# Kernel optimization log

Measured on AMD Instinct MI355X. Metric: run time of the kernel, lower is better.

## Reference

```python
import jax, jax.numpy as jnp
import numpy as np
import math

B, T, D, H, V = 32, 512, 256, 4, 5000
NL = 6          # transformer layers
DUR_CAP = 8     # cap per-token duration so output length is static under jit
T_OUT = 2048    # fixed regulated length (avg duration ~1-2 with small init)


def _layernorm(x, g, b, eps=1e-5):
    m = jnp.mean(x, axis=-1, keepdims=True)
    v = jnp.var(x, axis=-1, keepdims=True)
    return (x - m) * jax.lax.rsqrt(v + eps) * g + b


def _conv1d(x, w, b):
    # x [B,C,T], w [O,I,K] -> [B,O,T], 'same' padding as in torch
    pad = (w.shape[-1] - 1) // 2
    y = jax.lax.conv_general_dilated(x, w, (1,), [(pad, pad)],
                                     dimension_numbers=('NCH', 'OIH', 'NCH'))
    return y + b[None, :, None]


def _pos_encoding(t, d):
    pos = jnp.arange(t, dtype=jnp.float32)[:, None]
    div = jnp.exp(jnp.arange(0, d, 2, dtype=jnp.float32) * (-math.log(10000.0) / d))
    ang = pos * div  # [t, d/2]
    return jnp.stack([jnp.sin(ang), jnp.cos(ang)], axis=-1).reshape(t, d)


def setup_inputs():
    key = jax.random.key(0)
    ks = iter(jax.random.split(key, 64))
    def nrm(shape, s=0.02):
        return jax.random.normal(next(ks), shape, dtype=jnp.float32) * s
    return {
        'text': jax.random.randint(next(ks), (B, T), 0, V, dtype=jnp.int32),
        'emotion': jax.random.normal(next(ks), (B, 1), dtype=jnp.float32),
        'emb': nrm((V, D), 1.0),
        'Wqkv': nrm((NL, D, 3 * D)), 'bqkv': jnp.zeros((NL, 3 * D)),
        'Wo': nrm((NL, D, D)), 'bo': jnp.zeros((NL, D)),
        'W1': nrm((NL, D, 4 * D)), 'b1': jnp.zeros((NL, 4 * D)),
        'W2': nrm((NL, 4 * D, D)), 'b2': jnp.zeros((NL, D)),
        'ln1g': jnp.ones((NL, D)), 'ln1b': jnp.zeros((NL, D)),
        'ln2g': jnp.ones((NL, D)), 'ln2b': jnp.zeros((NL, D)),
        'We1': nrm((1, 64), 0.1), 'be1': jnp.zeros((64,)),
        'We2': nrm((64, D), 0.1), 'be2': jnp.zeros((D,)),
        'dp_w1': nrm((D, D, 3)), 'dp_b1': jnp.zeros((D,)),
        'dp_g1': jnp.ones((D,)), 'dp_bt1': jnp.zeros((D,)),
        'dp_m1': jnp.zeros((D,)), 'dp_v1': jnp.ones((D,)),
        'dp_w2': nrm((D, D, 3)), 'dp_b2': jnp.zeros((D,)),
        'dp_g2': jnp.ones((D,)), 'dp_bt2': jnp.zeros((D,)),
        'dp_m2': jnp.zeros((D,)), 'dp_v2': jnp.ones((D,)),
        'dp_wo': nrm((1, D, 1)), 'dp_bo': jnp.zeros((1,)),
        'dec_w1': nrm((256, D, 5)), 'dec_b1': jnp.zeros((256,)),
        'dec_w2': nrm((128, 256, 5)), 'dec_b2': jnp.zeros((128,)),
        'dec_w3': nrm((1, 128, 5)), 'dec_b3': jnp.zeros((1,)),
    }


def reference(text, emotion, emb, Wqkv, bqkv, Wo, bo, W1, b1, W2, b2,
              ln1g, ln1b, ln2g, ln2b, We1, be1, We2, be2,
              dp_w1, dp_b1, dp_g1, dp_bt1, dp_m1, dp_v1,
              dp_w2, dp_b2, dp_g2, dp_bt2, dp_m2, dp_v2, dp_wo, dp_bo,
              dec_w1, dec_b1, dec_w2, dec_b2, dec_w3, dec_b3):
    dh = D // H
    scale = 1.0 / math.sqrt(dh)
    x = emb[text] + _pos_encoding(T, D)[None]  # [B,T,D]
    # post-norm TransformerEncoder (torch default), relu FFN, eval mode
    for i in range(NL):
        qkv = x @ Wqkv[i] + bqkv[i]
        q, k, v = jnp.split(qkv, 3, axis=-1)
        q = q.reshape(B, T, H, dh); k = k.reshape(B, T, H, dh); v = v.reshape(B, T, H, dh)
        att = jax.nn.softmax(jnp.einsum('bthd,bshd->bhts', q, k) * scale, axis=-1)
        o = jnp.einsum('bhts,bshd->bthd', att, v).reshape(B, T, D) @ Wo[i] + bo[i]
        x = _layernorm(x + o, ln1g[i], ln1b[i])
        ff = jax.nn.relu(x @ W1[i] + b1[i]) @ W2[i] + b2[i]
        x = _layernorm(x + ff, ln2g[i], ln2b[i])
    # EmotionFusion (assumed additive MLP projection, output_dim = 256)
    e = jax.nn.relu(emotion @ We1 + be1) @ We2 + be2  # [B,256]
    fused = x + e[:, None, :]                          # [B,T,D]
    # DurationPredictor (eval: BN with running stats, dropout off)
    def bn(y, g, bt, m, vv):
        return g[None, :, None] * (y - m[None, :, None]) * jax.lax.rsqrt(vv + 1e-5)[None, :, None] + bt[None, :, None]
    h = fused.transpose(0, 2, 1)  # [B,D,T]
    h = bn(jax.nn.relu(_conv1d(h, dp_w1, dp_b1)), dp_g1, dp_bt1, dp_m1, dp_v1)
    h = bn(jax.nn.relu(_conv1d(h, dp_w2, dp_b2)), dp_g2, dp_bt2, dp_m2, dp_v2)
    log_dur = _conv1d(h, dp_wo, dp_bo)[:, 0, :]  # [B,T]
    dur = jnp.clip(jnp.round(jnp.exp(log_dur)), 1, DUR_CAP).astype(jnp.int32)
    dur = jax.lax.stop_gradient(dur)
    # LengthRegulator: repeat token i dur[i] times, zero-pad to T_OUT
    def regulate(xb, db):
        total = jnp.sum(db)
        pad = jnp.maximum(T_OUT - total, 0)
        xe = jnp.concatenate([xb, jnp.zeros((1, D), xb.dtype)], axis=0)
        de = jnp.concatenate([db, pad[None]], axis=0)
        return jnp.repeat(xe, de, axis=0, total_repeat_length=T_OUT)
    reg = jax.vmap(regulate)(fused, dur)  # [B,T_OUT,D]
    # decoder conv stack
    y = reg.transpose(0, 2, 1)
    y = jax.nn.relu(_conv1d(y, dec_w1, dec_b1))
    y = jax.nn.relu(_conv1d(y, dec_w2, dec_b2))
    wav = _conv1d(y, dec_w3, dec_b3)[:, 0, :]  # [B,T_OUT]
    return wav
```

## Files before the change

kernel.cpp:

```cpp
#include <hip/hip_runtime.h>
#include <math.h>

#define NB 32
#define NT 512
#define ND 256
#define NH 4
#define NLAYER 6
#define TOUT 2048

typedef __attribute__((ext_vector_type(8))) short bf16x8;
typedef __attribute__((ext_vector_type(4))) float f32x4;
typedef __attribute__((ext_vector_type(16))) float f32x16;

static __device__ __forceinline__ unsigned short f2b(float f) {
    union { float f; unsigned int u; } x; x.f = f;
    unsigned int u = x.u;
    return (unsigned short)((u + 0x7FFFu + ((u >> 16) & 1u)) >> 16);
}
static __device__ __forceinline__ float b2f(unsigned short s) {
    union { unsigned int u; float f; } x; x.u = ((unsigned int)s) << 16;
    return x.f;
}

#define OFF_X    0ull
#define OFF_FFH  4194304ull
#define OFF_WBT  12582912ull
#define OFF_CWT  14942208ull
#define OFF_QKV  20971520ull
#define OFF_ATTN 33554432ull
#define OFF_PROJ 37748736ull
#define OFF_E    41943040ull
#define OFF_INT  41951232ull

__global__ __launch_bounds__(256) void embed_kernel(const int* __restrict__ text,
                                                    const float* __restrict__ emb,
                                                    float* __restrict__ x)
{
    const int row = blockIdx.x;
    const int d = threadIdx.x;
    const int t = row & (NT - 1);
    const int id = text[row];
    const int j2 = (d >> 1) * 2;
    const float c = -9.210340371976184f / 256.0f;
    float freq = expf((float)j2 * c);
    float ang = (float)t * freq;
    float pe = (d & 1) ? cosf(ang) : sinf(ang);
    x[(size_t)row * ND + d] = emb[(size_t)id * ND + d] + pe;
}

__global__ __launch_bounds__(256) void wq_kernel(const float* __restrict__ W,
                                                 unsigned short* __restrict__ out,
                                                 int K, int N, int inLS, int outLS)
{
    __shared__ float tile[32][33];
    const float* Wl = W + (size_t)blockIdx.z * inLS;
    unsigned short* ol = out + (size_t)blockIdx.z * outLS;
    const int n0 = blockIdx.x * 32, k0 = blockIdx.y * 32;
    const int tx = threadIdx.x & 31, ty = threadIdx.x >> 5;
#pragma unroll
    for (int j = 0; j < 4; ++j)
        tile[ty + j * 8][tx] = Wl[(size_t)(k0 + ty + j * 8) * N + n0 + tx];
    __syncthreads();
#pragma unroll
    for (int j = 0; j < 4; ++j)
        ol[(size_t)(n0 + ty + j * 8) * K + k0 + tx] = f2b(tile[tx][ty + j * 8]);
}

template<int NTILE, bool RELU, bool ABF16, bool CBF16>
__global__ __launch_bounds__(256) void gemmbf_kernel(const void* __restrict__ A_,
                                                     const unsigned short* __restrict__ Bt,
                                                     const float* __restrict__ bias,
                                                     void* __restrict__ C_,
                                                     int M, int N, int K)
{
    constexpr int MT = (NTILE == 128) ? 2 : 1;
    __shared__ __align__(16) unsigned short Asb[128 * 32];
    __shared__ __align__(16) unsigned short Bsb[NTILE * 32];
    const int tid = threadIdx.x;
    const int lane = tid & 63, wave = tid >> 6;
    const int ln = lane & 31, hi = lane >> 5;
    const int row0 = blockIdx.y * 128, col0 = blockIdx.x * NTILE;
    const int mOff = (NTILE == 128) ? (wave >> 1) * 64 : wave * 32;
    const int nOff = (NTILE == 128) ? (wave & 1) * 64 : 0;
    const float* Af = (const float*)A_;
    const unsigned short* Ab = (const unsigned short*)A_;
    float* Cf = (float*)C_;
    unsigned short* Cb = (unsigned short*)C_;
    f32x16 acc[MT][2] = {};

    for (int k0 = 0; k0 < K; k0 += 32) {
#pragma unroll
        for (int it = 0; it < 2; ++it) {
            int u = it * 256 + tid;
            int m = u >> 2, blk = u & 3;
            unsigned short s8[8];
            if (ABF16) {
                *(uint4*)s8 = *(const uint4*)&Ab[(size_t)(row0 + m) * K + k0 + blk * 8];
            } else {
                float4 v0 = *(const float4*)&Af[(size_t)(row0 + m) * K + k0 + blk * 8];
                float4 v1 = *(const float4*)&Af[(size_t)(row0 + m) * K + k0 + blk * 8 + 4];
                s8[0] = f2b(v0.x); s8[1] = f2b(v0.y); s8[2] = f2b(v0.z); s8[3] = f2b(v0.w);
                s8[4] = f2b(v1.x); s8[5] = f2b(v1.y); s8[6] = f2b(v1.z); s8[7] = f2b(v1.w);
            }
            *(uint4*)&Asb[m * 32 + ((blk ^ (m & 3)) << 3)] = *(uint4*)s8;
        }
#pragma unroll
        for (int it = 0; it < NTILE / 64; ++it) {
            int u = it * 256 + tid;
            int n = u >> 2, blk = u & 3;
            *(uint4*)&Bsb[n * 32 + ((blk ^ (n & 3)) << 3)] =
                *(const uint4*)&Bt[(size_t)(col0 + n) * K + k0 + blk * 8];
        }
        __syncthreads();
#pragma unroll
        for (int kh = 0; kh < 2; ++kh) {
            const int kb = kh * 2 + hi;
            bf16x8 af[MT], bfr[2];
#pragma unroll
            for (int mt = 0; mt < MT; ++mt) {
                int r = mOff + mt * 32 + ln;
                af[mt] = *(const bf16x8*)&Asb[r * 32 + ((kb ^ (r & 3)) << 3)];
            }
#pragma unroll
            for (int nt = 0; nt < 2; ++nt) {
                int r = nOff + nt * 32 + ln;
                bfr[nt] = *(const bf16x8*)&Bsb[r * 32 + ((kb ^ (r & 3)) << 3)];
            }
#pragma unroll
            for (int mt = 0; mt < MT; ++mt)
#pragma unroll
                for (int nt = 0; nt < 2; ++nt)
                    acc[mt][nt] = __builtin_amdgcn_mfma_f32_32x32x16_bf16(
                        af[mt], bfr[nt], acc[mt][nt], 0, 0, 0);
        }
        __syncthreads();
    }
#pragma unroll
    for (int mt = 0; mt < MT; ++mt)
#pragma unroll
        for (int nt = 0; nt < 2; ++nt) {
            int col = col0 + nOff + nt * 32 + ln;
            float bi = bias[col];
#pragma unroll
            for (int g = 0; g < 4; ++g)
#pragma unroll
                for (int r4 = 0; r4 < 4; ++r4) {
                    int row = row0 + mOff + mt * 32 + hi * 4 + g * 8 + r4;
                    float v = acc[mt][nt][g * 4 + r4] + bi;
                    if (RELU) v = fmaxf(v, 0.f);
                    if (CBF16) Cb[(size_t)row * N + col] = f2b(v);
                    else       Cf[(size_t)row * N + col] = v;
                }
        }
}

__global__ __launch_bounds__(256) void vtrans_kernel(const unsigned short* __restrict__ qkv,
                                                     unsigned short* __restrict__ vt)
{
    __shared__ unsigned short tile[64][65];
    const int t0 = blockIdx.x * 64, h = blockIdx.y, b = blockIdx.z;
    const int tid = threadIdx.x;
#pragma unroll
    for (int it = 0; it < 2; ++it) {
        int u = it * 256 + tid;
        int t = u >> 3, d8 = (u & 7) * 8;
        bf16x8 v = *(const bf16x8*)&qkv[((size_t)(b * NT) + t0 + t) * 768 + 512 + h * 64 + d8];
#pragma unroll
        for (int j = 0; j < 8; ++j) tile[t][d8 + j] = (unsigned short)v[j];
    }
    __syncthreads();
#pragma unroll
    for (int it = 0; it < 2; ++it) {
        int u = it * 256 + tid;
        int d = u >> 3, t8 = (u & 7) * 8;
        unsigned short s8[8];
#pragma unroll
        for (int j = 0; j < 8; ++j) s8[j] = tile[t8 + j][d];
        *(uint4*)&vt[((size_t)(b * NH + h) * 64 + d) * NT + t0 + t8] = *(uint4*)s8;
    }
}

__global__ __launch_bounds__(256, 2) void attn3_kernel(const unsigned short* __restrict__ qkv,
                                                       const unsigned short* __restrict__ vt,
                                                       unsigned short* __restrict__ out)
{
    __shared__ __align__(16) unsigned short sP[4][32 * 64];
    const int tid = threadIdx.x;
    const int lane = tid & 63, wave = tid >> 6;
    const int ln = lane & 31, hi = lane >> 5;
    const int h = blockIdx.y, b = blockIdx.z;
    const int q0 = blockIdx.x * 128 + wave * 32;
    const size_t base = (size_t)b * NT * 768;
    const int qoff = h * 64;
    const unsigned short* vbh = vt + (size_t)(b * NH + h) * 64 * NT;

    bf16x8 qf[4];
#pragma unroll
    for (int s = 0; s < 4; ++s)
        qf[s] = *(const bf16x8*)&qkv[base + (size_t)(q0 + ln) * 768 + qoff + s * 16 + hi * 8];

    float mrow[16], lrow[16];
#pragma unroll
    for (int i = 0; i < 16; ++i) { mrow[i] = -1e30f; lrow[i] = 0.f; }
    f32x16 oacc[2] = {};
    const float sc = 0.18033688011112042f;
    const int i0 = (ln & 3) | (((ln >> 3) & 3) << 2);
    const bool own = (((ln >> 2) & 1) == hi);
    unsigned short* Pw = &sP[wave][0];

    for (int ch = 0; ch < 8; ++ch) {
        const int s0 = ch * 64;
        f32x16 sacc[2] = {};
#pragma unroll
        for (int ct = 0; ct < 2; ++ct)
#pragma unroll
            for (int s = 0; s < 4; ++s) {
                bf16x8 kf = *(const bf16x8*)&qkv[base + (size_t)(s0 + ct * 32 + ln) * 768
                                                 + 256 + qoff + s * 16 + hi * 8];
                sacc[ct] = __builtin_amdgcn_mfma_f32_32x32x16_bf16(qf[s], kf, sacc[ct], 0, 0, 0);
            }
        float alpha[16];
#pragma unroll
        for (int i = 0; i < 16; ++i) {
            float s20 = sacc[0][i] * sc, s21 = sacc[1][i] * sc;
            float mx = fmaxf(s20, s21);
#pragma unroll
            for (int o = 1; o < 32; o <<= 1) mx = fmaxf(mx, __shfl_xor(mx, o));
            float mn = fmaxf(mrow[i], mx);
            alpha[i] = exp2f(mrow[i] - mn);
            mrow[i] = mn;
            float p0 = exp2f(s20 - mn);
            float p1 = exp2f(s21 - mn);
            sacc[0][i] = p0; sacc[1][i] = p1;
            float rs = p0 + p1;
#pragma unroll
            for (int o = 1; o < 32; o <<= 1) rs += __shfl_xor(rs, o);
            lrow[i] = lrow[i] * alpha[i] + rs;
        }
#pragma unroll
        for (int ct = 0; ct < 2; ++ct) {
            int kb = ct * 4 + (ln >> 3), k7 = ln & 7;
#pragma unroll
            for (int i = 0; i < 16; ++i) {
                int q = (i & 3) + 8 * (i >> 2) + 4 * hi;
                Pw[q * 64 + (((kb ^ (q & 7)) << 3) | k7)] = f2b(sacc[ct][i]);
            }
        }
        __syncthreads();
        {
            float av = alpha[i0];
            float ao = __shfl_xor(av, 32);
            float aq = own ? av : ao;
#pragma unroll
            for (int ct = 0; ct < 2; ++ct)
#pragma unroll
                for (int i = 0; i < 16; ++i)
                    oacc[ct][i] *= aq;
        }
#pragma unroll
        for (int s = 0; s < 4; ++s) {
            bf16x8 pf = *(const bf16x8*)&Pw[ln * 64 + (((s * 2 + hi) ^ (ln & 7)) << 3)];
#pragma unroll
            for (int ct = 0; ct < 2; ++ct) {
                bf16x8 vf = *(const bf16x8*)&vbh[(size_t)(ct * 32 + ln) * NT + s0 + s * 16 + hi * 8];
                oacc[ct] = __builtin_amdgcn_mfma_f32_32x32x16_bf16(vf, pf, oacc[ct], 0, 0, 0);
            }
        }
        __syncthreads();
    }
    float lv = lrow[i0];
    float lo = __shfl_xor(lv, 32);
    float linv = 1.0f / (own ? lv : lo);
    const int q = q0 + ln;
#pragma unroll
    for (int ct = 0; ct < 2; ++ct)
#pragma unroll
        for (int i = 0; i < 16; ++i) {
            int d = ct * 32 + (i & 3) + 8 * (i >> 2) + 4 * hi;
            out[(size_t)(b * NT + q) * ND + qoff + d] = f2b(oacc[ct][i] * linv);
        }
}

__global__ __launch_bounds__(256) void add_ln_kernel(float* __restrict__ x,
                                                     const float* __restrict__ y,
                                                     const float* __restrict__ g,
                                                     const float* __restrict__ bta)
{
    const int w = threadIdx.x >> 6, lane = threadIdx.x & 63;
    const size_t row = (size_t)blockIdx.x * 4 + w;
    const int c4 = lane * 4;
    float4 xv = *(const float4*)&x[row * ND + c4];
    float4 yv = *(const float4*)&y[row * ND + c4];
    float4 v = make_float4(xv.x + yv.x, xv.y + yv.y, xv.z + yv.z, xv.w + yv.w);
    float s = v.x + v.y + v.z + v.w;
#pragma unroll
    for (int o = 1; o < 64; o <<= 1) s += __shfl_xor(s, o);
    float m = s * (1.0f / 256.0f);
    float4 dv = make_float4(v.x - m, v.y - m, v.z - m, v.w - m);
    float s2 = dv.x * dv.x + dv.y * dv.y + dv.z * dv.z + dv.w * dv.w;
#pragma unroll
    for (int o = 1; o < 64; o <<= 1) s2 += __shfl_xor(s2, o);
    float r = 1.0f / sqrtf(s2 * (1.0f / 256.0f) + 1e-5f);
    float4 gv = *(const float4*)&g[c4];
    float4 bv = *(const float4*)&bta[c4];
    float4 o4 = make_float4(dv.x * r * gv.x + bv.x, dv.y * r * gv.y + bv.y,
                            dv.z * r * gv.z + bv.z, dv.w * r * gv.w + bv.w);
    *(float4*)&x[row * ND + c4] = o4;
}

__global__ __launch_bounds__(256) void emotion_kernel(const float* __restrict__ emo,
                                                      const float* __restrict__ We1,
                                                      const float* __restrict__ be1,
                                                      const float* __restrict__ We2,
                                                      const float* __restrict__ be2,
                                                      float* __restrict__ e)
{
    const int b = blockIdx.x, d = threadIdx.x;
    const float em = emo[b];
    float acc = be2[d];
    for (int j = 0; j < 64; ++j) {
        float h = fmaxf(em * We1[j] + be1[j], 0.0f);
        acc = fmaf(h, We2[j * ND + d], acc);
    }
    e[b * ND + d] = acc;
}

__global__ __launch_bounds__(256) void addfuse_kernel(float* __restrict__ x,
                                                      const float* __restrict__ e)
{
    const int row = blockIdx.x;
    const int d = threadIdx.x;
    x[(size_t)row * ND + d] += e[(row >> 9) * ND + d];
}

__global__ __launch_bounds__(256) void wtrans_kernel(const float* __restrict__ w,
                                                     float* __restrict__ wt,
                                                     int CIN, int COUT, int KS)
{
    int gid = blockIdx.x * 256 + threadIdx.x;
    int total = CIN * COUT * KS;
    if (gid >= total) return;
    int o = gid % COUT;
    int r = gid / COUT;
    int c = r % CIN;
    int k = r / CIN;
    wt[gid] = w[(o * CIN + c) * KS + k];
}

__global__ __launch_bounds__(256) void wtransb_kernel(const float* __restrict__ w,
                                                      unsigned short* __restrict__ wtb,
                                                      int CIN, int COUT, int KS)
{
    int gid = blockIdx.x * 256 + threadIdx.x;
    int total = CIN * COUT * KS;
    if (gid >= total) return;
    int c = gid % CIN;
    int r = gid / CIN;
    int o = r % COUT;
    int k = r / COUT;
    wtb[gid] = f2b(w[(o * CIN + c) * KS + k]);
}

template<int CIN, int KS, bool RELU, bool BN, bool GATHER>
__global__ __launch_bounds__(256, 4) void convg_kernel(const float* __restrict__ in,
                                                       const float* __restrict__ wt,
                                                       const float* __restrict__ bias,
                                                       const float* __restrict__ bng,
                                                       const float* __restrict__ bnb,
                                                       const float* __restrict__ bnm,
                                                       const float* __restrict__ bnv,
                                                       const int* __restrict__ tok,
                                                       float* __restrict__ out,
                                                       int T, int in_T, int COUT)
{
    constexpr int TM = 128;
    constexpr int PAD = (KS - 1) / 2;
    constexpr int TEXT = TM + KS - 1;
    constexpr int PITCH = (TEXT + 3) & ~3;
    __shared__ __align__(16) float As[16 * PITCH];
    __shared__ __align__(16) float Bs[16 * KS * 68];
    const int tid = threadIdx.x;
    const int lane = tid & 63, wave = tid >> 6;
    const int b = blockIdx.z;
    const int t0 = blockIdx.x * TM;
    const int o0 = blockIdx.y * 64;
    const int wt0 = wave * 32;
    const int r0 = (lane >> 3) << 2;
    const int c0 = (lane & 7) << 2;
    float acc[4][8] = {};

    for (int cc = 0; cc < CIN; cc += 16) {
        for (int i = tid; i < TEXT * 4; i += 256) {
            int t = i >> 2, q = i & 3;
            int tg = t0 - PAD + t;
            float4 v = make_float4(0.f, 0.f, 0.f, 0.f);
            if (tg >= 0 && tg < T) {
                long row;
                if (GATHER) {
                    int tk = tok[b * T + tg];
                    row = (tk >= 0) ? ((long)b * in_T + tk) : -1;
                } else {
                    row = (long)b * T + tg;
                }
                if (row >= 0) v = *(const float4*)&in[row * CIN + cc + (q << 2)];
            }
            As[((q << 2) + 0) * PITCH + t] = v.x;
            As[((q << 2) + 1) * PITCH + t] = v.y;
            As[((q << 2) + 2) * PITCH + t] = v.z;
            As[((q << 2) + 3) * PITCH + t] = v.w;
        }
        for (int i = tid; i < KS * 256; i += 256) {
            int row = i >> 4, o4 = (i & 15) << 2;
            int k = row >> 4, ci = row & 15;
            *(float4*)&Bs[row * 68 + o4] =
                *(const float4*)&wt[(size_t)(k * CIN + cc + ci) * COUT + o0 + o4];
        }
        __syncthreads();
#pragma unroll 2
        for (int ci = 0; ci < 16; ++ci) {
            float a[8];
            float4 A0 = *(const float4*)&As[ci * PITCH + wt0 + r0];
            float4 A1 = *(const float4*)&As[ci * PITCH + wt0 + r0 + 4];
            a[0] = A0.x; a[1] = A0.y; a[2] = A0.z; a[3] = A0.w;
            a[4] = A1.x; a[5] = A1.y; a[6] = A1.z; a[7] = A1.w;
#pragma unroll
            for (int k = 0; k < KS; ++k) {
                float4 b0 = *(const float4*)&Bs[(k * 16 + ci) * 68 + c0];
                float4 b1 = *(const float4*)&Bs[(k * 16 + ci) * 68 + 32 + c0];
                float bb[8] = {b0.x, b0.y, b0.z, b0.w, b1.x, b1.y, b1.z, b1.w};
#pragma unroll
                for (int i = 0; i < 4; ++i)
#pragma unroll
                    for (int j = 0; j < 8; ++j)
                        acc[i][j] = fmaf(a[i + k], bb[j], acc[i][j]);
            }
        }
        __syncthreads();
    }

    float4 bi0 = *(const float4*)(bias + o0 + c0);
    float4 bi1 = *(const float4*)(bias + o0 + 32 + c0);
    float bb[8] = {bi0.x, bi0.y, bi0.z, bi0.w, bi1.x, bi1.y, bi1.z, bi1.w};
    float sc[8], sh[8];
    if (BN) {
        float4 g0 = *(const float4*)(bng + o0 + c0);
        float4 g1 = *(const float4*)(bng + o0 + 32 + c0);
        float4 t0v = *(const float4*)(bnb + o0 + c0);
        float4 t1v = *(const float4*)(bnb + o0 + 32 + c0);
        float4 m0 = *(const float4*)(bnm + o0 + c0);
        float4 m1 = *(const float4*)(bnm + o0 + 32 + c0);
        float4 v0 = *(const float4*)(bnv + o0 + c0);
        float4 v1 = *(const float4*)(bnv + o0 + 32 + c0);
        float gg[8] = {g0.x, g0.y, g0.z, g0.w, g1.x, g1.y, g1.z, g1.w};
        float tb[8] = {t0v.x, t0v.y, t0v.z, t0v.w, t1v.x, t1v.y, t1v.z, t1v.w};
        float mm[8] = {m0.x, m0.y, m0.z, m0.w, m1.x, m1.y, m1.z, m1.w};
        float vv[8] = {v0.x, v0.y, v0.z, v0.w, v1.x, v1.y, v1.z, v1.w};
#pragma unroll
        for (int j = 0; j < 8; ++j) {
            sc[j] = gg[j] / sqrtf(vv[j] + 1e-5f);
            sh[j] = tb[j] - mm[j] * sc[j];
        }
    }
#pragma unroll
    for (int i = 0; i < 4; ++i) {
        int r = t0 + wt0 + r0 + i;
#pragma unroll
        for (int jh = 0; jh < 2; ++jh) {
            float o4[4];
#pragma unroll
            for (int j = 0; j < 4; ++j) {
                float yv = acc[i][jh * 4 + j] + bb[jh * 4 + j];
                if (RELU) yv = fmaxf(yv, 0.0f);
                if (BN) yv = yv * sc[jh * 4 + j] + sh[jh * 4 + j];
                o4[j] = yv;
            }
            *(float4*)&out[((size_t)b * T + r) * COUT + o0 + jh * 32 + c0] =
                make_float4(o4[0], o4[1], o4[2], o4[3]);
        }
    }
}

template<int CIN, int KS, bool GATHER, bool IN_BF16>
__global__ __launch_bounds__(256) void convmf_kernel(const void* __restrict__ in_,
                                                     const unsigned short* __restrict__ wtb,
                                                     const float* __restrict__ bias,
                                                     const int* __restrict__ tok,
                                                     unsigned short* __restrict__ out,
                                                     int T, int in_T, int COUT)
{
    constexpr int TM = 256;
    constexpr int PAD = (KS - 1) / 2;
    constexpr int TEXT = TM + KS - 1;
    constexpr int PITCHA = 40;
    __shared__ __align__(16) unsigned short As[TEXT * PITCHA];
    const int tid = threadIdx.x;
    const int lane = tid & 63, wave = tid >> 6;
    const int m = lane & 15, quad = lane >> 4;
    const int b = blockIdx.z;
    const int t0 = blockIdx.x * TM;
    const int o0 = blockIdx.y * 64;
    const int woff = wave * 64;
    f32x4 acc[4][4] = {};

    const float* inf = (const float*)in_;
    const unsigned short* inb = (const unsigned short*)in_;

    for (int cc = 0; cc < CIN; cc += 32) {
        for (int i = tid; i < TEXT * 8; i += 256) {
            int t = i >> 3, ci4 = (i & 7) << 2;
            int tg = t0 - PAD + t;
            long row = -1;
            if (tg >= 0 && tg < T) {
                if (GATHER) {
                    int tk = tok[b * T + tg];
                    if (tk >= 0) row = (long)b * in_T + tk;
                } else {
                    row = (long)b * T + tg;
                }
            }
            unsigned short s4[4] = {0, 0, 0, 0};
            if (row >= 0) {
                if (IN_BF16) {
                    *(uint2*)s4 = *(const uint2*)&inb[row * CIN + cc + ci4];
                } else {
                    float4 v = *(const float4*)&inf[row * CIN + cc + ci4];
                    s4[0] = f2b(v.x); s4[1] = f2b(v.y);
                    s4[2] = f2b(v.z); s4[3] = f2b(v.w);
                }
            }
            *(uint2*)&As[t * PITCHA + ci4] = *(uint2*)s4;
        }
        __syncthreads();
#pragma unroll
        for (int tap = 0; tap < KS; ++tap) {
            bf16x8 a[4];
#pragma unroll
            for (int mt = 0; mt < 4; ++mt)
                a[mt] = *(const bf16x8*)&As[(woff + mt * 16 + m + tap) * PITCHA + quad * 8];
#pragma unroll
            for (int ot = 0; ot < 4; ++ot) {
                bf16x8 bf = *(const bf16x8*)&wtb[((size_t)tap * COUT + o0 + ot * 16 + m) * CIN + cc + quad * 8];
#pragma unroll
                for (int mt = 0; mt < 4; ++mt)
                    acc[mt][ot] = __builtin_amdgcn_mfma_f32_16x16x32_bf16(a[mt], bf, acc[mt][ot], 0, 0, 0);
            }
        }
        __syncthreads();
    }

#pragma unroll
    for (int ot = 0; ot < 4; ++ot) {
        int o = o0 + ot * 16 + m;
        float bi = bias[o];
#pragma unroll
        for (int mt = 0; mt < 4; ++mt)
#pragma unroll
            for (int r = 0; r < 4; ++r) {
                int t = t0 + woff + mt * 16 + quad * 4 + r;
                float yv = fmaxf(acc[mt][ot][r] + bi, 0.0f);
                out[((size_t)b * T + t) * COUT + o] = f2b(yv);
            }
    }
}

__global__ __launch_bounds__(256) void dur_kernel(const float* __restrict__ h2,
                                                  const float* __restrict__ wo,
                                                  const float* __restrict__ bo,
                                                  int* __restrict__ dur)
{
    __shared__ float red[4];
    const int row = blockIdx.x;
    const int c = threadIdx.x;
    float s = h2[(size_t)row * ND + c] * wo[c];
#pragma unroll
    for (int o = 32; o; o >>= 1) s += __shfl_down(s, o);
    if ((c & 63) == 0) red[c >> 6] = s;
    __syncthreads();
    if (c == 0) {
        float ld = red[0] + red[1] + red[2] + red[3] + bo[0];
        float d = rintf(expf(ld));
        d = fminf(fmaxf(d, 1.0f), 8.0f);
        dur[row] = (int)d;
    }
}

__global__ __launch_bounds__(64) void scan_kernel(const int* __restrict__ dur,
                                                  int* __restrict__ starts,
                                                  int* __restrict__ totals)
{
    const int b = threadIdx.x;
    if (b >= NB) return;
    int acc = 0;
    for (int t = 0; t < NT; ++t) {
        starts[b * NT + t] = acc;
        acc += dur[b * NT + t];
    }
    totals[b] = acc;
}

__global__ __launch_bounds__(256) void tok_kernel(const int* __restrict__ starts,
                                                  const int* __restrict__ totals,
                                                  int* __restrict__ tok)
{
    const int gid = blockIdx.x * 256 + threadIdx.x;
    const int b = gid >> 11, p = gid & (TOUT - 1);
    const int total = totals[b];
    int res = -1;
    if (p < total) {
        const int* st = starts + b * NT;
        int lo = 0, hi = NT - 1;
        while (lo < hi) {
            int mid = (lo + hi + 1) >> 1;
            if (st[mid] <= p) lo = mid; else hi = mid - 1;
        }
        res = lo;
    }
    tok[gid] = res;
}

__global__ __launch_bounds__(256) void conv3_kernel(const unsigned short* __restrict__ in,
                                                    const float* __restrict__ w,
                                                    const float* __restrict__ bias,
                                                    float* __restrict__ out)
{
    const int gid = blockIdx.x * 256 + threadIdx.x;
    const int b = gid >> 11, t = gid & (TOUT - 1);
    float acc = bias[0];
#pragma unroll
    for (int k = 0; k < 5; ++k) {
        int t2 = t + k - 2;
        if (t2 < 0 || t2 >= TOUT) continue;
        const unsigned short* row = in + ((size_t)b * TOUT + t2) * 128;
        for (int c = 0; c < 128; ++c) acc = fmaf(b2f(row[c]), w[c * 5 + k], acc);
    }
    out[gid] = acc;
}

extern "C" void kernel_launch(void* const* d_in, const int* in_sizes, int n_in,
                              void* d_out, int out_size, void* d_ws, size_t ws_size,
                              hipStream_t stream)
{
    const int*   text    = (const int*)d_in[0];
    const float* emotion = (const float*)d_in[1];
    const float* emb     = (const float*)d_in[2];
    const float* Wqkv    = (const float*)d_in[3];
    const float* bqkv    = (const float*)d_in[4];
    const float* Wo      = (const float*)d_in[5];
    const float* bo      = (const float*)d_in[6];
    const float* W1      = (const float*)d_in[7];
    const float* b1      = (const float*)d_in[8];
    const float* W2      = (const float*)d_in[9];
    const float* b2      = (const float*)d_in[10];
    const float* ln1g    = (const float*)d_in[11];
    const float* ln1b    = (const float*)d_in[12];
    const float* ln2g    = (const float*)d_in[13];
    const float* ln2b    = (const float*)d_in[14];
    const float* We1     = (const float*)d_in[15];
    const float* be1     = (const float*)d_in[16];
    const float* We2     = (const float*)d_in[17];
    const float* be2     = (const float*)d_in[18];
    const float* dp_w1   = (const float*)d_in[19];
    const float* dp_b1   = (const float*)d_in[20];
    const float* dp_g1   = (const float*)d_in[21];
    const float* dp_bt1  = (const float*)d_in[22];
    const float* dp_m1   = (const float*)d_in[23];
    const float* dp_v1   = (const float*)d_in[24];
    const float* dp_w2   = (const float*)d_in[25];
    const float* dp_b2   = (const float*)d_in[26];
    const float* dp_g2   = (const float*)d_in[27];
    const float* dp_bt2  = (const float*)d_in[28];
    const float* dp_m2   = (const float*)d_in[29];
    const float* dp_v2   = (const float*)d_in[30];
    const float* dp_wo   = (const float*)d_in[31];
    const float* dp_bo   = (const float*)d_in[32];
    const float* dec_w1  = (const float*)d_in[33];
    const float* dec_b1  = (const float*)d_in[34];
    const float* dec_w2  = (const float*)d_in[35];
    const float* dec_b2  = (const float*)d_in[36];
    const float* dec_w3  = (const float*)d_in[37];
    const float* dec_b3  = (const float*)d_in[38];

    float* ws   = (float*)d_ws;
    float* x    = ws + OFF_X;
    unsigned short* ffhB = (unsigned short*)(ws + OFF_FFH);
    unsigned short* Wbt  = (unsigned short*)(ws + OFF_WBT);
    float* wtdp1 = ws + OFF_CWT;
    float* wtdp2 = wtdp1 + 196608;
    unsigned short* wtb1 = (unsigned short*)(wtdp2 + 196608);
    unsigned short* wtb2 = wtb1 + 327680;
    unsigned short* qkvB = (unsigned short*)(ws + OFF_QKV);
    unsigned short* vtb  = qkvB + 12582912;
    float* attb = ws + OFF_ATTN;
    float* prjb = ws + OFF_PROJ;
    float* ebuf = ws + OFF_E;
    unsigned short* attbB = (unsigned short*)attb;
    unsigned short* d1b  = ffhB;
    unsigned short* d2b  = (unsigned short*)attb;
    int*   ip     = (int*)(ws + OFF_INT);
    int*   durb   = ip;
    int*   startb = ip + 16384;
    int*   totb   = ip + 32768;
    int*   tokb   = ip + 32832;

    const int M = NB * NT;

    embed_kernel<<<M, 256, 0, stream>>>(text, emb, x);

    wq_kernel<<<dim3(24, 8, 6), 256, 0, stream>>>(Wqkv, Wbt + 0,      256, 768,  196608, 786432);
    wq_kernel<<<dim3(8,  8, 6), 256, 0, stream>>>(Wo,   Wbt + 196608, 256, 256,  65536,  786432);
    wq_kernel<<<dim3(32, 8, 6), 256, 0, stream>>>(W1,   Wbt + 262144, 256, 1024, 262144, 786432);
    wq_kernel<<<dim3(8, 32, 6), 256, 0, stream>>>(W2,   Wbt + 524288, 1024, 256, 262144, 786432);

    for (int l = 0; l < NLAYER; ++l) {
        const unsigned short* WQ  = Wbt + (size_t)l * 786432;
        const unsigned short* WO  = WQ + 196608;
        const unsigned short* WF1 = WQ + 262144;
        const unsigned short* WF2 = WQ + 524288;
        gemmbf_kernel<128, false, false, true><<<dim3(6, 128), 256, 0, stream>>>(
            x, WQ, bqkv + l * 768, qkvB, M, 768, 256);
        vtrans_kernel<<<dim3(NT / 64, NH, NB), 256, 0, stream>>>(qkvB, vtb);
        attn3_kernel<<<dim3(NT / 128, NH, NB), 256, 0, stream>>>(qkvB, vtb, attbB);
        gemmbf_kernel<64, false, true, false><<<dim3(4, 128), 256, 0, stream>>>(
            attbB, WO, bo + l * 256, prjb, M, 256, 256);
        add_ln_kernel<<<M / 4, 256, 0, stream>>>(x, prjb, ln1g + l * ND, ln1b + l * ND);
        gemmbf_kernel<128, true, false, true><<<dim3(8, 128), 256, 0, stream>>>(
            x, WF1, b1 + l * 1024, ffhB, M, 1024, 256);
        gemmbf_kernel<64, false, true, false><<<dim3(4, 128), 256, 0, stream>>>(
            ffhB, WF2, b2 + l * 256, prjb, M, 256, 1024);
        add_ln_kernel<<<M / 4, 256, 0, stream>>>(x, prjb, ln2g + l * ND, ln2b + l * ND);
    }

    emotion_kernel<<<NB, 256, 0, stream>>>(emotion, We1, be1, We2, be2, ebuf);
    addfuse_kernel<<<M, 256, 0, stream>>>(x, ebuf);

    wtrans_kernel<<<(256 * 256 * 3 + 255) / 256, 256, 0, stream>>>(dp_w1, wtdp1, 256, 256, 3);
    wtrans_kernel<<<(256 * 256 * 3 + 255) / 256, 256, 0, stream>>>(dp_w2, wtdp2, 256, 256, 3);
    wtransb_kernel<<<(256 * 256 * 5 + 255) / 256, 256, 0, stream>>>(dec_w1, wtb1, 256, 256, 5);
    wtransb_kernel<<<(128 * 256 * 5 + 255) / 256, 256, 0, stream>>>(dec_w2, wtb2, 256, 128, 5);

    convg_kernel<256, 3, true, true, false><<<dim3(NT / 128, 4, NB), 256, 0, stream>>>(
        x, wtdp1, dp_b1, dp_g1, dp_bt1, dp_m1, dp_v1, nullptr, attb, NT, NT, 256);
    convg_kernel<256, 3, true, true, false><<<dim3(NT / 128, 4, NB), 256, 0, stream>>>(
        attb, wtdp2, dp_b2, dp_g2, dp_bt2, dp_m2, dp_v2, nullptr, prjb, NT, NT, 256);
    dur_kernel<<<M, 256, 0, stream>>>(prjb, dp_wo, dp_bo, durb);
    scan_kernel<<<1, 64, 0, stream>>>(durb, startb, totb);
    tok_kernel<<<NB * TOUT / 256, 256, 0, stream>>>(startb, totb, tokb);

    convmf_kernel<256, 5, true, false><<<dim3(TOUT / 256, 4, NB), 256, 0, stream>>>(
        x, wtb1, dec_b1, tokb, d1b, TOUT, NT, 256);
    convmf_kernel<256, 5, false, true><<<dim3(TOUT / 256, 2, NB), 256, 0, stream>>>(
        d1b, wtb2, dec_b2, nullptr, d2b, TOUT, TOUT, 128);
    conv3_kernel<<<NB * TOUT / 256, 256, 0, stream>>>(d2b, dec_w3, dec_b3, (float*)d_out);
}
```

Baseline: 1.689 ms.

## Restructure decoder convs: separate regulate gather, 32x32 MFMA with LDS-staged weights

Moves the length-regulator gather into its own kernel that writes a bf16 regulated buffer. The decoder convs then use a new kernel that stages both activations and weights in XOR-swizzled LDS and runs 32x32x16 MFMAs over 128-row tiles, instead of reading weights straight from global memory per tap. The duration and final 1-channel conv kernels are rewritten to use one wave per row with vector loads and shuffle reductions, replacing the serial per-thread 640-term loop in conv3. This costs an extra buffer round trip for the regulated activations and adds more blocks.

```diff
diff --git a/kernel.cpp b/kernel.cpp
--- a/kernel.cpp
+++ b/kernel.cpp
@@ -480,85 +480,92 @@
     }
 }
 
-template<int CIN, int KS, bool GATHER, bool IN_BF16>
-__global__ __launch_bounds__(256) void convmf_kernel(const void* __restrict__ in_,
-                                                     const unsigned short* __restrict__ wtb,
-                                                     const float* __restrict__ bias,
-                                                     const int* __restrict__ tok,
-                                                     unsigned short* __restrict__ out,
-                                                     int T, int in_T, int COUT)
-{
-    constexpr int TM = 256;
+__global__ __launch_bounds__(256) void reg_kernel(const float* __restrict__ x,
+                                                  const int* __restrict__ tok,
+                                                  unsigned short* __restrict__ reg)
+{
+    const int wave = threadIdx.x >> 6, lane = threadIdx.x & 63;
+    const int row = blockIdx.x * 4 + wave;
+    const int tk = tok[row];
+    const int b = row >> 11;
+    const int c4 = lane * 4;
+    unsigned short s4[4] = {0, 0, 0, 0};
+    if (tk >= 0) {
+        float4 v = *(const float4*)&x[((size_t)(b * NT) + tk) * ND + c4];
+        s4[0] = f2b(v.x); s4[1] = f2b(v.y); s4[2] = f2b(v.z); s4[3] = f2b(v.w);
+    }
+    *(uint2*)&reg[(size_t)row * ND + c4] = *(uint2*)s4;
+}
+
+template<int CIN, int KS, bool RELU>
+__global__ __launch_bounds__(256) void convmf2_kernel(const unsigned short* __restrict__ in,
+                                                      const unsigned short* __restrict__ wtb,
+                                                      const float* __restrict__ bias,
+                                                      unsigned short* __restrict__ out,
+                                                      int T, int COUT)
+{
     constexpr int PAD = (KS - 1) / 2;
-    constexpr int TEXT = TM + KS - 1;
-    constexpr int PITCHA = 40;
-    __shared__ __align__(16) unsigned short As[TEXT * PITCHA];
+    constexpr int TEXT = 128 + KS - 1;
+    __shared__ __align__(16) unsigned short Asb[TEXT * 32];
+    __shared__ __align__(16) unsigned short Bsb[KS * 64 * 32];
     const int tid = threadIdx.x;
     const int lane = tid & 63, wave = tid >> 6;
-    const int m = lane & 15, quad = lane >> 4;
+    const int ln = lane & 31, hi = lane >> 5;
     const int b = blockIdx.z;
-    const int t0 = blockIdx.x * TM;
+    const int t0 = blockIdx.x * 128;
     const int o0 = blockIdx.y * 64;
-    const int woff = wave * 64;
-    f32x4 acc[4][4] = {};
-
-    const float* inf = (const float*)in_;
-    const unsigned short* inb = (const unsigned short*)in_;
+    const int mOff = wave * 32;
+    f32x16 acc[2] = {};
 
     for (int cc = 0; cc < CIN; cc += 32) {
-        for (int i = tid; i < TEXT * 8; i += 256) {
-            int t = i >> 3, ci4 = (i & 7) << 2;
+        for (int u = tid; u < TEXT * 4; u += 256) {
+            int t = u >> 2, blk = u & 3;
             int tg = t0 - PAD + t;
-            long row = -1;
-            if (tg >= 0 && tg < T) {
-                if (GATHER) {
-                    int tk = tok[b * T + tg];
-                    if (tk >= 0) row = (long)b * in_T + tk;
-                } else {
-                    row = (long)b * T + tg;
+            uint4 v = make_uint4(0, 0, 0, 0);
+            if (tg >= 0 && tg < T)
+                v = *(const uint4*)&in[((size_t)(b * T) + tg) * CIN + cc + blk * 8];
+            *(uint4*)&Asb[t * 32 + ((blk ^ (t & 3)) << 3)] = v;
+        }
+        for (int u = tid; u < KS * 256; u += 256) {
+            int row = u >> 2, blk = u & 3;
+            int k = row >> 6, o = row & 63;
+            *(uint4*)&Bsb[row * 32 + ((blk ^ (row & 3)) << 3)] =
+                *(const uint4*)&wtb[((size_t)k * COUT + o0 + o) * CIN + cc + blk * 8];
+        }
+        __syncthreads();
+#pragma unroll
+        for (int kh = 0; kh < 2; ++kh) {
+            const int kb = kh * 2 + hi;
+            bf16x8 af[KS];
+#pragma unroll
+            for (int tap = 0; tap < KS; ++tap) {
+                int r = mOff + ln + tap;
+                af[tap] = *(const bf16x8*)&Asb[r * 32 + ((kb ^ (r & 3)) << 3)];
+            }
+#pragma unroll
+            for (int nt = 0; nt < 2; ++nt) {
+                int rb = nt * 32 + ln;
+#pragma unroll
+                for (int tap = 0; tap < KS; ++tap) {
+                    bf16x8 bfr = *(const bf16x8*)&Bsb[(tap * 64 + rb) * 32 + ((kb ^ (rb & 3)) << 3)];
+                    acc[nt] = __builtin_amdgcn_mfma_f32_32x32x16_bf16(af[tap], bfr, acc[nt], 0, 0, 0);
                 }
             }
-            unsigned short s4[4] = {0, 0, 0, 0};
-            if (row >= 0) {
-                if (IN_BF16) {
-                    *(uint2*)s4 = *(const uint2*)&inb[row * CIN + cc + ci4];
-                } else {
-                    float4 v = *(const float4*)&inf[row * CIN + cc + ci4];
-                    s4[0] = f2b(v.x); s4[1] = f2b(v.y);
-                    s4[2] = f2b(v.z); s4[3] = f2b(v.w);
-                }
-            }
-            *(uint2*)&As[t * PITCHA + ci4] = *(uint2*)s4;
         }
         __syncthreads();
-#pragma unroll
-        for (int tap = 0; tap < KS; ++tap) {
-            bf16x8 a[4];
-#pragma unroll
-            for (int mt = 0; mt < 4; ++mt)
-                a[mt] = *(const bf16x8*)&As[(woff + mt * 16 + m + tap) * PITCHA + quad * 8];
-#pragma unroll
-            for (int ot = 0; ot < 4; ++ot) {
-                bf16x8 bf = *(const bf16x8*)&wtb[((size_t)tap * COUT + o0 + ot * 16 + m) * CIN + cc + quad * 8];
-#pragma unroll
-                for (int mt = 0; mt < 4; ++mt)
-                    acc[mt][ot] = __builtin_amdgcn_mfma_f32_16x16x32_bf16(a[mt], bf, acc[mt][ot], 0, 0, 0);
-            }
-        }
-        __syncthreads();
-    }
-
-#pragma unroll
-    for (int ot = 0; ot < 4; ++ot) {
-        int o = o0 + ot * 16 + m;
-        float bi = bias[o];
-#pragma unroll
-        for (int mt = 0; mt < 4; ++mt)
-#pragma unroll
-            for (int r = 0; r < 4; ++r) {
-                int t = t0 + woff + mt * 16 + quad * 4 + r;
-                float yv = fmaxf(acc[mt][ot][r] + bi, 0.0f);
-                out[((size_t)b * T + t) * COUT + o] = f2b(yv);
+    }
+#pragma unroll
+    for (int nt = 0; nt < 2; ++nt) {
+        int col = o0 + nt * 32 + ln;
+        float bi = bias[col];
+#pragma unroll
+        for (int g = 0; g < 4; ++g)
+#pragma unroll
+            for (int r4 = 0; r4 < 4; ++r4) {
+                int row = t0 + mOff + hi * 4 + g * 8 + r4;
+                float v = acc[nt][g * 4 + r4] + bi;
+                if (RELU) v = fmaxf(v, 0.f);
+                out[((size_t)(b * T) + row) * COUT + col] = f2b(v);
             }
     }
 }
@@ -568,17 +575,16 @@
                                                   const float* __restrict__ bo,
                                                   int* __restrict__ dur)
 {
-    __shared__ float red[4];
-    const int row = blockIdx.x;
-    const int c = threadIdx.x;
-    float s = h2[(size_t)row * ND + c] * wo[c];
-#pragma unroll
-    for (int o = 32; o; o >>= 1) s += __shfl_down(s, o);
-    if ((c & 63) == 0) red[c >> 6] = s;
-    __syncthreads();
-    if (c == 0) {
-        float ld = red[0] + red[1] + red[2] + red[3] + bo[0];
-        float d = rintf(expf(ld));
+    const int wave = threadIdx.x >> 6, lane = threadIdx.x & 63;
+    const int row = blockIdx.x * 4 + wave;
+    const int c4 = lane * 4;
+    float4 h = *(const float4*)&h2[(size_t)row * ND + c4];
+    float4 w4 = *(const float4*)&wo[c4];
+    float s = h.x * w4.x + h.y * w4.y + h.z * w4.z + h.w * w4.w;
+#pragma unroll
+    for (int o = 1; o < 64; o <<= 1) s += __shfl_xor(s, o);
+    if (lane == 0) {
+        float d = rintf(expf(s + bo[0]));
         d = fminf(fmaxf(d, 1.0f), 8.0f);
         dur[row] = (int)d;
     }
@@ -623,17 +629,25 @@
                                                     const float* __restrict__ bias,
                                                     float* __restrict__ out)
 {
-    const int gid = blockIdx.x * 256 + threadIdx.x;
+    const int wave = threadIdx.x >> 6, lane = threadIdx.x & 63;
+    const int gid = blockIdx.x * 4 + wave;
     const int b = gid >> 11, t = gid & (TOUT - 1);
-    float acc = bias[0];
+    const int c = lane * 2;
+    float w0[5], w1[5];
+#pragma unroll
+    for (int k = 0; k < 5; ++k) { w0[k] = w[c * 5 + k]; w1[k] = w[(c + 1) * 5 + k]; }
+    float acc = 0.f;
 #pragma unroll
     for (int k = 0; k < 5; ++k) {
         int t2 = t + k - 2;
         if (t2 < 0 || t2 >= TOUT) continue;
-        const unsigned short* row = in + ((size_t)b * TOUT + t2) * 128;
-        for (int c = 0; c < 128; ++c) acc = fmaf(b2f(row[c]), w[c * 5 + k], acc);
-    }
-    out[gid] = acc;
+        unsigned int u = *(const unsigned int*)&in[((size_t)(b * TOUT) + t2) * 128 + c];
+        acc = fmaf(b2f((unsigned short)(u & 0xFFFF)), w0[k], acc);
+        acc = fmaf(b2f((unsigned short)(u >> 16)), w1[k], acc);
+    }
+#pragma unroll
+    for (int o = 1; o < 64; o <<= 1) acc += __shfl_xor(acc, o);
+    if (lane == 0) out[gid] = acc + bias[0];
 }
 
 extern "C" void kernel_launch(void* const* d_in, const int* in_sizes, int n_in,
@@ -690,6 +704,7 @@
     unsigned short* wtb2 = wtb1 + 327680;
     unsigned short* qkvB = (unsigned short*)(ws + OFF_QKV);
     unsigned short* vtb  = qkvB + 12582912;
+    unsigned short* regB = qkvB;
     float* attb = ws + OFF_ATTN;
     float* prjb = ws + OFF_PROJ;
     float* ebuf = ws + OFF_E;
@@ -742,13 +757,14 @@
         x, wtdp1, dp_b1, dp_g1, dp_bt1, dp_m1, dp_v1, nullptr, attb, NT, NT, 256);
     convg_kernel<256, 3, true, true, false><<<dim3(NT / 128, 4, NB), 256, 0, stream>>>(
         attb, wtdp2, dp_b2, dp_g2, dp_bt2, dp_m2, dp_v2, nullptr, prjb, NT, NT, 256);
-    dur_kernel<<<M, 256, 0, stream>>>(prjb, dp_wo, dp_bo, durb);
+    dur_kernel<<<M / 4, 256, 0, stream>>>(prjb, dp_wo, dp_bo, durb);
     scan_kernel<<<1, 64, 0, stream>>>(durb, startb, totb);
     tok_kernel<<<NB * TOUT / 256, 256, 0, stream>>>(startb, totb, tokb);
 
-    convmf_kernel<256, 5, true, false><<<dim3(TOUT / 256, 4, NB), 256, 0, stream>>>(
-        x, wtb1, dec_b1, tokb, d1b, TOUT, NT, 256);
-    convmf_kernel<256, 5, false, true><<<dim3(TOUT / 256, 2, NB), 256, 0, stream>>>(
-        d1b, wtb2, dec_b2, nullptr, d2b, TOUT, TOUT, 128);
-    conv3_kernel<<<NB * TOUT / 256, 256, 0, stream>>>(d2b, dec_w3, dec_b3, (float*)d_out);
-}
+    reg_kernel<<<NB * TOUT / 4, 256, 0, stream>>>(x, tokb, regB);
+    convmf2_kernel<256, 5, true><<<dim3(TOUT / 128, 4, NB), 256, 0, stream>>>(
+        regB, wtb1, dec_b1, d1b, TOUT, 256);
+    convmf2_kernel<256, 5, true><<<dim3(TOUT / 128, 2, NB), 256, 0, stream>>>(
+        d1b, wtb2, dec_b2, d2b, TOUT, 128);
+    conv3_kernel<<<NB * TOUT / 4, 256, 0, stream>>>(d2b, dec_w3, dec_b3, (float*)d_out);
+}
```

Result: faster. 1.619 ms (-4.1%).
